# Kernel tuning notes

Measured on AMD Instinct MI355X. Metric: run time of the kernel, lower is better.

Reference implementation:

```python
import jax, jax.numpy as jnp
import numpy as np
from jax import lax

C = 128      # channels
H = 128
W = 128
B = 2
WS = 4       # window size
HEADS = 4
HID = int(C * 2.66)  # 340
EPS = 1e-6


def conv1x1(x, w):
    # x: [b,c,h,w], w: [out,in]
    return jnp.einsum('oc,bchw->bohw', w, x)


def dwconv3(x, w):
    # depthwise 3x3, w: [c,1,3,3]
    return lax.conv_general_dilated(
        x, w, window_strides=(1, 1), padding='SAME',
        feature_group_count=x.shape[1],
        dimension_numbers=('NCHW', 'OIHW', 'NCHW'))


def layernorm(x, w, b):
    # channel-wise LN over dim 1 (per pixel), w/b: [C]
    m = x.mean(axis=1, keepdims=True)
    v = ((x - m) ** 2).mean(axis=1, keepdims=True)
    xn = (x - m) / jnp.sqrt(v + EPS)
    return xn * w[None, :, None, None] + b[None, :, None, None]


def l2norm(x):
    n = jnp.sqrt(jnp.sum(x * x, axis=-1, keepdims=True))
    return x / jnp.maximum(n, 1e-12)


def rsa(x, qkv_w, dw_w, proj_w, temp):
    b, c, h, w = x.shape
    ws = WS
    x_ = jnp.roll(x, (-ws // 2, -ws // 2), axis=(2, 3))  # shifts > 0
    qkv = dwconv3(conv1x1(x_, qkv_w), dw_w)
    q, k, v = jnp.split(qkv, 3, axis=1)

    def win(t):  # b c (h dh) (w dw) -> b (h w) (dh dw) c
        return t.reshape(b, c, h // ws, ws, w // ws, ws) \
                .transpose(0, 2, 4, 3, 5, 1) \
                .reshape(b, (h // ws) * (w // ws), ws * ws, c)

    q, k, v = win(q), win(k), win(v)
    q = l2norm(q)
    k = l2norm(k)
    # attn = q^T @ k  -> [b, nw, c, c]
    attn = jax.nn.relu(jnp.einsum('bnpc,bnpd->bncd', q, k) * temp[0, 0, 0])
    out = jnp.einsum('bnpc,bncd->bnpd', v, attn)  # v @ attn
    out = out.reshape(b, h // ws, w // ws, ws, ws, c) \
             .transpose(0, 5, 1, 3, 2, 4).reshape(b, c, h, w)
    out = jnp.roll(out, (ws // 2, ws // 2), axis=(2, 3))
    return conv1x1(out, proj_w)


def gsa(x, qkv_w, dw_w, proj_w, temp):
    b, c, h, w = x.shape
    hd = HEADS
    ch = c // hd
    qkv = dwconv3(conv1x1(x, qkv_w), dw_w)
    q, k, v = jnp.split(qkv, 3, axis=1)

    def hs(t):  # b (head c) h w -> b head c (h w)
        return t.reshape(b, hd, ch, h * w)

    q, k, v = hs(q), hs(k), hs(v)
    q = l2norm(q)
    k = l2norm(k)
    attn = jax.nn.relu(jnp.einsum('bhcn,bhdn->bhcd', q, k) * temp[0, 0, 0])
    out = jnp.einsum('bhcd,bhdn->bhcn', attn, v).reshape(b, c, h, w)
    return conv1x1(out, proj_w)


def ffn(x, w_in, w_dw, w_out):
    h = dwconv3(conv1x1(x, w_in), w_dw)
    h = jax.nn.gelu(h, approximate=False)
    return conv1x1(h, w_out)


def setup_inputs() -> dict:
    key = jax.random.key(0)
    ks = jax.random.split(key, 16)
    s = 0.05
    d = {
        'x': jax.random.normal(ks[0], (B, C, H, W), jnp.float32),
        # spatial (RSA) branch
        'w_s0': jnp.ones((C,), jnp.float32), 'b_s0': jnp.zeros((C,), jnp.float32),
        'w_s2': jnp.ones((C,), jnp.float32), 'b_s2': jnp.zeros((C,), jnp.float32),
        'rsa_qkv': jax.random.normal(ks[1], (3 * C, C), jnp.float32) * s,
        'rsa_dw': jax.random.normal(ks[2], (3 * C, 1, 3, 3), jnp.float32) * s,
        'rsa_proj': jax.random.normal(ks[3], (C, C), jnp.float32) * s,
        'rsa_temp': jnp.ones((1, 1, 1), jnp.float32),
        'ffs_in': jax.random.normal(ks[4], (HID, C), jnp.float32) * s,
        'ffs_dw': jax.random.normal(ks[5], (HID, 1, 3, 3), jnp.float32) * s,
        'ffs_out': jax.random.normal(ks[6], (C, HID), jnp.float32) * s,
        # channel (GSA) branch
        'w_c0': jnp.ones((C,), jnp.float32), 'b_c0': jnp.zeros((C,), jnp.float32),
        'w_c2': jnp.ones((C,), jnp.float32), 'b_c2': jnp.zeros((C,), jnp.float32),
        'gsa_qkv': jax.random.normal(ks[7], (3 * C, C), jnp.float32) * s,
        'gsa_dw': jax.random.normal(ks[8], (3 * C, 1, 3, 3), jnp.float32) * s,
        'gsa_proj': jax.random.normal(ks[9], (C, C), jnp.float32) * s,
        'gsa_temp': jnp.ones((1, 1, 1), jnp.float32),
        'ffc_in': jax.random.normal(ks[10], (HID, C), jnp.float32) * s,
        'ffc_dw': jax.random.normal(ks[11], (HID, 1, 3, 3), jnp.float32) * s,
        'ffc_out': jax.random.normal(ks[12], (C, HID), jnp.float32) * s,
    }
    return d


def reference(x, w_s0, b_s0, w_s2, b_s2, rsa_qkv, rsa_dw, rsa_proj, rsa_temp,
              ffs_in, ffs_dw, ffs_out,
              w_c0, b_c0, w_c2, b_c2, gsa_qkv, gsa_dw, gsa_proj, gsa_temp,
              ffc_in, ffc_dw, ffc_out):
    # shared_depth = 1: only the i==0 branches execute
    # spatial block (RSA)
    x_ = rsa(layernorm(x, w_s0, b_s0), rsa_qkv, rsa_dw, rsa_proj, rsa_temp)
    x = ffn(layernorm(x_ + x, w_s2, b_s2), ffs_in, ffs_dw, ffs_out) + x_
    # channel block (GSA)
    x_ = gsa(layernorm(x, w_c0, b_c0), gsa_qkv, gsa_dw, gsa_proj, gsa_temp)
    x = ffn(layernorm(x_ + x, w_c2, b_c2), ffc_in, ffc_dw, ffc_out) + x_
    return x
```

## Files before the change

### kernel.cpp

```cpp
#include <hip/hip_runtime.h>
#include <hip/hip_bf16.h>
#include <math.h>

typedef __hip_bfloat16 bf16;
typedef __attribute__((ext_vector_type(8))) short short8;
typedef __attribute__((ext_vector_type(4))) short short4v;
typedef __attribute__((ext_vector_type(4))) float float4v;

static constexpr int cB  = 2;
static constexpr int cC  = 128;
static constexpr int cH  = 128;
static constexpr int cW  = 128;
static constexpr int cP  = cH * cW;
static constexpr int cC3 = 384;
static constexpr int cHID = 340;
static constexpr int cNW = 1024;
static constexpr float cEPS = 1e-6f;

__device__ __forceinline__ float bfu2f(unsigned short u){
  union { unsigned int i; float f; } c; c.i = ((unsigned int)u) << 16; return c.f;
}
__device__ __forceinline__ unsigned short f2b(float f){
  union { float f; unsigned int u; } c; c.f = f;
  unsigned int r = c.u + 0x7FFFu + ((c.u >> 16) & 1u);
  return (unsigned short)(r >> 16);
}

__global__ void k_wcvt(const float* __restrict__ qkv_s, const float* __restrict__ qkv_c,
                       const float* __restrict__ fin_s, const float* __restrict__ fin_c,
                       const float* __restrict__ prj_s, const float* __restrict__ prj_c,
                       const float* __restrict__ fo_s,  const float* __restrict__ fo_c,
                       unsigned short* __restrict__ WB, float* __restrict__ S){
  int i = blockIdx.x * 256 + threadIdx.x;
  if (i >= 319488){
    int j = i - 319488;
    if (j < 8704) S[j] = 0.f;
    return;
  }
  float v;
  if (i < 98304){
    v = (i < 49152) ? qkv_s[i] : qkv_c[i - 49152];
  } else if (i < 196608){
    int j = (i < 147456) ? (i - 98304) : (i - 147456);
    int row = j >> 7, col = j & 127;
    const float* src = (i < 147456) ? fin_s : fin_c;
    v = (row < cHID) ? src[row * 128 + col] : 0.f;
  } else if (i < 229376){
    v = (i < 212992) ? prj_s[i - 196608] : prj_c[i - 212992];
  } else {
    int j = (i < 274432) ? (i - 229376) : (i - 274432);
    int row = j / 352, col = j - row * 352;
    const float* src = (i < 274432) ? fo_s : fo_c;
    v = (col < cHID) ? src[row * cHID + col] : 0.f;
  }
  WB[i] = f2b(v);
}

__global__ void __launch_bounds__(256) k_gemmLN(const unsigned short* __restrict__ Wb,
                                                const float* __restrict__ Xf,
                                                const float* __restrict__ gamma,
                                                const float* __restrict__ beta,
                                                unsigned short* __restrict__ Out){
  __shared__ short Xls[64 * 136];
  __shared__ short Wls[128 * 40];
  __shared__ float gls[128], bls[128];
  __shared__ float psum[64], pssq[64];
  int bid = blockIdx.x;
  int s  = (bid & 7) * 192 + (bid >> 3);
  int mt = s % 3;
  int r3 = s / 3;
  int pt = r3 & 255;
  int b  = r3 >> 8;
  int p0 = pt * 64;
  int m0 = mt * 128;
  int t  = threadIdx.x;
  int px = t & 63, cq = t >> 6;
  if (t < 64){ psum[t] = 0.f; pssq[t] = 0.f; }
  if (t < 128){ gls[t] = gamma[t]; bls[t] = beta[t]; }
  int rh = p0 >> 7, w0 = p0 & 127;
  int hs = (rh + 2) & (cH - 1);
  int sp = hs * cW + ((w0 + 2 + px) & (cW - 1));
  const float* xb = Xf + (size_t)b * cC * cP + sp;
  float xr[32];
  float s1 = 0.f, s2 = 0.f;
  #pragma unroll
  for (int j = 0; j < 32; j++){
    float v = xb[(size_t)(cq * 32 + j) * cP];
    xr[j] = v; s1 += v; s2 += v * v;
  }
  __syncthreads();
  atomicAdd(&psum[px], s1);
  atomicAdd(&pssq[px], s2);
  __syncthreads();
  float mean = psum[px] * (1.f / cC);
  float var  = pssq[px] * (1.f / cC) - mean * mean;
  float rstd = rsqrtf(var + cEPS);
  #pragma unroll
  for (int k = 0; k < 4; k++){
    short8 tv;
    #pragma unroll
    for (int e = 0; e < 8; e++){
      int c = cq * 32 + k * 8 + e;
      tv[e] = (short)f2b((xr[k * 8 + e] - mean) * rstd * gls[c] + bls[c]);
    }
    *(short8*)&Xls[px * 136 + cq * 32 + k * 8] = tv;
  }
  int lanelo = t & 15;
  int quad   = (t >> 4) & 3;
  int wv = t >> 6;
  int w1 = wv & 1;
  int w2 = wv >> 1;
  int srw = t >> 1;
  int kow = (t & 1) * 16;
  float4v acc[2][4];
  #pragma unroll
  for (int i = 0; i < 2; i++)
    #pragma unroll
    for (int j = 0; j < 4; j++)
      acc[i][j] = (float4v){0.f, 0.f, 0.f, 0.f};
  const unsigned short* Wp = Wb + (size_t)(m0 + srw) * 128 + kow;
  short8 a0 = *(const short8*)(Wp);
  short8 a1 = *(const short8*)(Wp + 8);
  for (int k0 = 0; k0 < 128; k0 += 32){
    __syncthreads();
    *(short8*)&Wls[srw * 40 + kow]     = a0;
    *(short8*)&Wls[srw * 40 + kow + 8] = a1;
    __syncthreads();
    if (k0 < 96){
      a0 = *(const short8*)(Wp + k0 + 32);
      a1 = *(const short8*)(Wp + k0 + 40);
    }
    short8 af[2], bfr[4];
    #pragma unroll
    for (int i = 0; i < 2; i++)
      af[i] = *(const short8*)&Xls[(w1 * 32 + i * 16 + lanelo) * 136 + k0 + quad * 8];
    #pragma unroll
    for (int j = 0; j < 4; j++)
      bfr[j] = *(const short8*)&Wls[(w2 * 64 + j * 16 + lanelo) * 40 + quad * 8];
    #pragma unroll
    for (int i = 0; i < 2; i++)
      #pragma unroll
      for (int j = 0; j < 4; j++)
        acc[i][j] = __builtin_amdgcn_mfma_f32_16x16x32_bf16(af[i], bfr[j], acc[i][j], 0, 0, 0);
  }
  __syncthreads();
  #pragma unroll
  for (int i = 0; i < 2; i++)
    #pragma unroll
    for (int j = 0; j < 4; j++){
      int pixloc = w1 * 32 + i * 16 + quad * 4;
      int mloc   = w2 * 64 + j * 16 + lanelo;
      #pragma unroll
      for (int r = 0; r < 4; r++)
        Xls[(pixloc + r) * 136 + mloc] = (short)f2b(acc[i][j][r]);
    }
  __syncthreads();
  unsigned short* Ob = Out + (size_t)b * cP * cC3;
  #pragma unroll
  for (int rr = 0; rr < 4; rr++){
    int id = t + rr * 256;
    int row = id >> 4, col8 = (id & 15) * 8;
    *(short8*)(Ob + (size_t)(p0 + row) * cC3 + m0 + col8) = *(const short8*)&Xls[row * 136 + col8];
  }
}

template<int MODE>
__global__ void __launch_bounds__(256) k_gfuse(const unsigned short* __restrict__ W1,
                                               const unsigned short* __restrict__ Xg,
                                               const float* __restrict__ R,
                                               const float* __restrict__ Base,
                                               const float* __restrict__ gamma,
                                               const float* __restrict__ beta,
                                               float* __restrict__ Tr,
                                               const unsigned short* __restrict__ W2,
                                               unsigned short* __restrict__ Out2,
                                               int K1, int PK1, int PITCH2, int M2LIM){
  __shared__ short XB[64 * 136];
  __shared__ short OB[64 * 136];
  __shared__ float gls[128], bls[128];
  __shared__ float psum[64], pssq[64];
  int b  = blockIdx.z;
  int p0 = blockIdx.x * 64;
  int t  = threadIdx.x;
  int lanelo = t & 15;
  int quad   = (t >> 4) & 3;
  int wv = t >> 6;
  int w2 = wv >> 1, w1 = wv & 1;

  if (t < 128){ gls[t] = gamma[t]; bls[t] = beta[t]; }
  if (t < 64){ psum[t] = 0.f; pssq[t] = 0.f; }

  float4v acc[4][2];
  #pragma unroll
  for (int i = 0; i < 4; i++){
    acc[i][0] = (float4v){0.f, 0.f, 0.f, 0.f};
    acc[i][1] = (float4v){0.f, 0.f, 0.f, 0.f};
  }
  const unsigned short* Wf[4];
  const unsigned short* Xf2[2];
  #pragma unroll
  for (int i = 0; i < 4; i++)
    Wf[i] = W1 + (size_t)(w2 * 64 + i * 16 + lanelo) * K1 + quad * 8;
  #pragma unroll
  for (int j = 0; j < 2; j++)
    Xf2[j] = Xg + (size_t)b * cP * PK1 + (size_t)(p0 + w1 * 32 + j * 16 + lanelo) * PK1 + quad * 8;
  #pragma unroll 2
  for (int k0 = 0; k0 < K1; k0 += 32){
    short8 af[4], bfr[2];
    #pragma unroll
    for (int i = 0; i < 4; i++)
      af[i] = *(const short8*)(Wf[i] + k0);
    #pragma unroll
    for (int j = 0; j < 2; j++)
      bfr[j] = *(const short8*)(Xf2[j] + k0);
    #pragma unroll
    for (int i = 0; i < 4; i++)
      #pragma unroll
      for (int j = 0; j < 2; j++)
        acc[i][j] = __builtin_amdgcn_mfma_f32_16x16x32_bf16(af[i], bfr[j], acc[i][j], 0, 0, 0);
  }
  float lnv[4][2][4];
  #pragma unroll
  for (int i = 0; i < 4; i++)
    #pragma unroll
    for (int j = 0; j < 2; j++){
      int n = p0 + w1 * 32 + j * 16 + lanelo;
      #pragma unroll
      for (int r = 0; r < 4; r++){
        int m = w2 * 64 + i * 16 + quad * 4 + r;
        size_t idx = (size_t)b * cC * cP + (size_t)m * cP + n;
        float v = acc[i][j][r];
        if (MODE == 2) v += R[idx];
        Tr[idx] = v;
        if (MODE == 1) v += Base[idx];
        lnv[i][j][r] = v;
      }
    }
  __syncthreads();
  #pragma unroll
  for (int j = 0; j < 2; j++){
    int nl = w1 * 32 + j * 16 + lanelo;
    float s = 0.f, ss = 0.f;
    #pragma unroll
    for (int i = 0; i < 4; i++)
      #pragma unroll
      for (int r = 0; r < 4; r++){
        float v = lnv[i][j][r];
        s += v; ss += v * v;
      }
    atomicAdd(&psum[nl], s);
    atomicAdd(&pssq[nl], ss);
  }
  __syncthreads();
  #pragma unroll
  for (int j = 0; j < 2; j++){
    int nl = w1 * 32 + j * 16 + lanelo;
    float mean = psum[nl] * (1.f / cC);
    float var = pssq[nl] * (1.f / cC) - mean * mean;
    float rstd = rsqrtf(var + cEPS);
    #pragma unroll
    for (int i = 0; i < 4; i++)
      #pragma unroll
      for (int r = 0; r < 4; r++){
        int m = w2 * 64 + i * 16 + quad * 4 + r;
        XB[nl * 136 + m] = (short)f2b((lnv[i][j][r] - mean) * rstd * gls[m] + bls[m]);
      }
  }
  __syncthreads();
  unsigned short* Ob = Out2 + (size_t)b * cP * PITCH2;
  for (int mc = 0; mc < 3; mc++){
    float4v a2[2][4];
    #pragma unroll
    for (int i = 0; i < 2; i++)
      #pragma unroll
      for (int j = 0; j < 4; j++)
        a2[i][j] = (float4v){0.f, 0.f, 0.f, 0.f};
    #pragma unroll
    for (int k0 = 0; k0 < 128; k0 += 32){
      short8 af2[2], bf2[4];
      #pragma unroll
      for (int i = 0; i < 2; i++)
        af2[i] = *(const short8*)&XB[(w1 * 32 + i * 16 + lanelo) * 136 + k0 + quad * 8];
      #pragma unroll
      for (int j = 0; j < 4; j++)
        bf2[j] = *(const short8*)(W2 + (size_t)(mc * 128 + w2 * 64 + j * 16 + lanelo) * 128 + k0 + quad * 8);
      #pragma unroll
      for (int i = 0; i < 2; i++)
        #pragma unroll
        for (int j = 0; j < 4; j++)
          a2[i][j] = __builtin_amdgcn_mfma_f32_16x16x32_bf16(af2[i], bf2[j], a2[i][j], 0, 0, 0);
    }
    __syncthreads();
    #pragma unroll
    for (int i = 0; i < 2; i++)
      #pragma unroll
      for (int j = 0; j < 4; j++){
        int pixloc = w1 * 32 + i * 16 + quad * 4;
        int mloc   = w2 * 64 + j * 16 + lanelo;
        #pragma unroll
        for (int r = 0; r < 4; r++)
          OB[(pixloc + r) * 136 + mloc] = (short)f2b(a2[i][j][r]);
      }
    __syncthreads();
    #pragma unroll
    for (int rr = 0; rr < 4; rr++){
      int id = t + rr * 256;
      int row = id >> 4, col8 = (id & 15) * 8;
      int wcol = mc * 128 + col8;
      if (wcol < M2LIM)
        *(short8*)(Ob + (size_t)(p0 + row) * PITCH2 + wcol) = *(const short8*)&OB[row * 136 + col8];
    }
  }
}

__global__ void __launch_bounds__(256) k_g64d3(const unsigned short* __restrict__ Wb,
                                               const unsigned short* __restrict__ Xg,
                                               const float* __restrict__ R,
                                               float* __restrict__ Tr,
                                               int K, int PK){
  int b  = blockIdx.z;
  int p0 = blockIdx.x * 64;
  int t  = threadIdx.x;
  int lanelo = t & 15;
  int quad   = (t >> 4) & 3;
  int wv = t >> 6;
  int w2 = wv >> 1, w1 = wv & 1;

  float4v acc[4][2];
  #pragma unroll
  for (int i = 0; i < 4; i++){
    acc[i][0] = (float4v){0.f, 0.f, 0.f, 0.f};
    acc[i][1] = (float4v){0.f, 0.f, 0.f, 0.f};
  }
  const unsigned short* Wf[4];
  const unsigned short* Xf2[2];
  #pragma unroll
  for (int i = 0; i < 4; i++)
    Wf[i] = Wb + (size_t)(w2 * 64 + i * 16 + lanelo) * K + quad * 8;
  #pragma unroll
  for (int j = 0; j < 2; j++)
    Xf2[j] = Xg + (size_t)b * cP * PK + (size_t)(p0 + w1 * 32 + j * 16 + lanelo) * PK + quad * 8;
  #pragma unroll 2
  for (int k0 = 0; k0 < K; k0 += 32){
    short8 af[4], bfr[2];
    #pragma unroll
    for (int i = 0; i < 4; i++)
      af[i] = *(const short8*)(Wf[i] + k0);
    #pragma unroll
    for (int j = 0; j < 2; j++)
      bfr[j] = *(const short8*)(Xf2[j] + k0);
    #pragma unroll
    for (int i = 0; i < 4; i++)
      #pragma unroll
      for (int j = 0; j < 2; j++)
        acc[i][j] = __builtin_amdgcn_mfma_f32_16x16x32_bf16(af[i], bfr[j], acc[i][j], 0, 0, 0);
  }
  #pragma unroll
  for (int i = 0; i < 4; i++)
    #pragma unroll
    for (int j = 0; j < 2; j++){
      int n = p0 + w1 * 32 + j * 16 + lanelo;
      #pragma unroll
      for (int r = 0; r < 4; r++){
        int m = w2 * 64 + i * 16 + quad * 4 + r;
        size_t idx = (size_t)b * cC * cP + (size_t)m * cP + n;
        Tr[idx] = acc[i][j][r] + R[idx];
      }
    }
}

template<int GELU, int CCn, int PITCH>
__global__ void __launch_bounds__(256) k_dw(const unsigned short* __restrict__ in,
                                            const float* __restrict__ wt,
                                            unsigned short* __restrict__ out){
  __shared__ float wls[16 * 76];
  int t = threadIdx.x;
  int cbase = blockIdx.y * 128;
  for (int i = t; i < 16 * 72; i += 256){
    int cg = i / 72, rem = i - cg * 72;
    int tap = rem >> 3, j = rem & 7;
    int c = cbase + cg * 8 + j;
    wls[cg * 76 + rem] = (c < CCn) ? wt[c * 9 + tap] : 0.f;
  }
  __syncthreads();
  int cgl = t & 15, pixl = t >> 4;
  int c0 = cbase + cgl * 8;
  if (c0 >= PITCH) return;
  int p = blockIdx.x * 16 + pixl;
  int h = p >> 7, w = p & 127;
  int b = blockIdx.z;
  const unsigned short* ib = in + (size_t)b * cP * PITCH;
  float4 wreg[18];
  #pragma unroll
  for (int q = 0; q < 18; q++)
    wreg[q] = *(const float4*)&wls[cgl * 76 + q * 4];
  short8 v[9];
  #pragma unroll
  for (int ky = 0; ky < 3; ky++){
    int hh = h + ky - 1;
    bool okh = (unsigned)hh < (unsigned)cH;
    int hc = okh ? hh : h;
    #pragma unroll
    for (int kx = 0; kx < 3; kx++){
      int ww = w + kx - 1;
      bool okw = (unsigned)ww < (unsigned)cW;
      int wc = okw ? ww : w;
      short8 lv = *(const short8*)(ib + (size_t)(hc * cW + wc) * PITCH + c0);
      if (!(okh && okw)) lv = (short8){0,0,0,0,0,0,0,0};
      v[ky * 3 + kx] = lv;
    }
  }
  float acc[8] = {0,0,0,0,0,0,0,0};
  #pragma unroll
  for (int tap = 0; tap < 9; tap++){
    float4 w0 = wreg[tap * 2];
    float4 w1 = wreg[tap * 2 + 1];
    float wa[8] = {w0.x, w0.y, w0.z, w0.w, w1.x, w1.y, w1.z, w1.w};
    #pragma unroll
    for (int j = 0; j < 8; j++)
      acc[j] += wa[j] * bfu2f((unsigned short)v[tap][j]);
  }
  short8 ov;
  #pragma unroll
  for (int j = 0; j < 8; j++){
    float vv = acc[j];
    if (GELU) vv = 0.5f * vv * (1.f + erff(vv * 0.70710678118654752f));
    ov[j] = (short)f2b(vv);
  }
  *(short8*)(out + (size_t)b * cP * PITCH + (size_t)p * PITCH + c0) = ov;
}

__global__ void __launch_bounds__(256) k_rsadw(const unsigned short* __restrict__ qkv,
                                               const float* __restrict__ wt,
                                               const float* __restrict__ temp,
                                               unsigned short* __restrict__ out){
  constexpr int QT = 0;
  constexpr int KT = 5120;
  constexpr int VO = 10240;
  constexpr int HA = 12416;
  constexpr int AT = 12416;
  __shared__ short lds[26528];
  __shared__ float nq[16], nk[16];
  int blk = blockIdx.x;
  int b  = blk >> 10;
  int nw = blk & 1023;
  int hb = nw >> 5, wb = nw & 31;
  int t = threadIdx.x;
  #pragma unroll
  for (int j = 0; j < 5; j++)
    *(short8*)&lds[t * 40 + j * 8] = (short8){0,0,0,0,0,0,0,0};
  if (t < 16) nq[t] = 0.f;
  else if (t < 32) nk[t - 16] = 0.f;
  __syncthreads();
  const unsigned short* base = qkv + (size_t)b * cP * cC3;
  #pragma unroll
  for (int r = 0; r < 7; r++){
    int i = t + 256 * r;
    if (i < 1728){
      int pix6 = i / 48;
      int cg = i - pix6 * 48;
      int hy = pix6 / 6, wx = pix6 - hy * 6;
      int hh = hb * 4 + hy - 1;
      int ww = wb * 4 + wx - 1;
      short8 v = (short8){0,0,0,0,0,0,0,0};
      if ((unsigned)hh < (unsigned)cH && (unsigned)ww < (unsigned)cW)
        v = *(const short8*)(base + (size_t)(hh * cW + ww) * cC3 + cg * 8);
      *(short8*)&lds[HA + pix6 * 392 + cg * 8] = v;
    }
  }
  __syncthreads();
  {
    int px = t & 15, grp = t >> 4;
    int py = px >> 2, pw = px & 3;
    #pragma unroll
    for (int g = 0; g < 3; g++){
      int c0 = grp * 24 + g * 8;
      const float4* wq = (const float4*)(wt + (size_t)c0 * 9);
      float wa[72];
      #pragma unroll
      for (int q = 0; q < 18; q++){
        float4 v4 = wq[q];
        wa[q * 4 + 0] = v4.x; wa[q * 4 + 1] = v4.y;
        wa[q * 4 + 2] = v4.z; wa[q * 4 + 3] = v4.w;
      }
      float acc8[8] = {0,0,0,0,0,0,0,0};
      #pragma unroll
      for (int ky = 0; ky < 3; ky++)
        #pragma unroll
        for (int kx = 0; kx < 3; kx++){
          short8 iv = *(const short8*)&lds[HA + ((py + ky) * 6 + pw + kx) * 392 + c0];
          int tap = ky * 3 + kx;
          #pragma unroll
          for (int e = 0; e < 8; e++)
            acc8[e] += wa[e * 9 + tap] * bfu2f((unsigned short)iv[e]);
        }
      if (c0 < 256){
        int isQ = c0 < 128;
        int off = isQ ? (QT + c0 * 40) : (KT + (c0 - 128) * 40);
        float s = 0.f;
        #pragma unroll
        for (int e = 0; e < 8; e++){
          unsigned short us = f2b(acc8[e]);
          float f = bfu2f(us);
          s += f * f;
          lds[off + e * 40 + px] = (short)us;
        }
        atomicAdd(isQ ? &nq[px] : &nk[px], s);
      } else {
        short8 sv;
        #pragma unroll
        for (int e = 0; e < 8; e++) sv[e] = (short)f2b(acc8[e]);
        *(short8*)&lds[VO + px * 136 + (c0 - 256)] = sv;
      }
    }
  }
  __syncthreads();
  float T = temp[0];
  #pragma unroll
  for (int r = 0; r < 8; r++){
    int idx = t + 256 * r;
    int c = idx >> 4, p = idx & 15;
    float sc = (1.f / fmaxf(sqrtf(nq[p]), 1e-12f)) * (1.f / fmaxf(sqrtf(nk[p]), 1e-12f));
    int a = QT + c * 40 + p;
    lds[a] = (short)f2b(bfu2f((unsigned short)lds[a]) * sc);
  }
  __syncthreads();
  int lanelo = t & 15;
  int quad = (t >> 4) & 3;
  int wv = t >> 6;
  float4v oacc[2];
  oacc[0] = (float4v){0.f,0.f,0.f,0.f};
  oacc[1] = (float4v){0.f,0.f,0.f,0.f};
  for (int ch = 0; ch < 2; ch++){
    #pragma unroll
    for (int ct = 0; ct < 4; ct++){
      int c0 = ch * 64 + ct * 16;
      short8 af = *(const short8*)&lds[QT + (c0 + lanelo) * 40 + quad * 8];
      #pragma unroll
      for (int dt = 0; dt < 2; dt++){
        int d0 = wv * 32 + dt * 16;
        short8 bf = *(const short8*)&lds[KT + (d0 + lanelo) * 40 + quad * 8];
        float4v acc = __builtin_amdgcn_mfma_f32_16x16x32_bf16(af, bf,
                        (float4v){0.f,0.f,0.f,0.f}, 0, 0, 0);
        short4v sv;
        #pragma unroll
        for (int r2 = 0; r2 < 4; r2++) sv[r2] = (short)f2b(fmaxf(acc[r2] * T, 0.f));
        *(short4v*)&lds[AT + (d0 + lanelo) * 72 + ct * 16 + quad * 4] = sv;
      }
    }
    __syncthreads();
    #pragma unroll
    for (int dt = 0; dt < 2; dt++){
      int d0 = wv * 32 + dt * 16;
      #pragma unroll
      for (int kk = 0; kk < 2; kk++){
        short8 av8 = *(const short8*)&lds[VO + lanelo * 136 + ch * 64 + kk * 32 + quad * 8];
        short8 bv8 = *(const short8*)&lds[AT + (d0 + lanelo) * 72 + kk * 32 + quad * 8];
        oacc[dt] = __builtin_amdgcn_mfma_f32_16x16x32_bf16(av8, bv8, oacc[dt], 0, 0, 0);
      }
    }
    __syncthreads();
  }
  #pragma unroll
  for (int dt = 0; dt < 2; dt++){
    int d = wv * 32 + dt * 16 + lanelo;
    #pragma unroll
    for (int r2 = 0; r2 < 4; r2++){
      int p = quad * 4 + r2;
      lds[p * 136 + d] = (short)f2b(oacc[dt][r2]);
    }
  }
  __syncthreads();
  {
    int px = t >> 4, cg = (t & 15) * 8;
    int h2 = (hb * 4 + (px >> 2) + 2) & (cH - 1);
    int w2 = (wb * 4 + (px & 3) + 2) & (cW - 1);
    short8 sv = *(const short8*)&lds[px * 136 + cg];
    *(short8*)(out + (size_t)b * cP * cC + (size_t)(h2 * cW + w2) * cC + cg) = sv;
  }
}

__global__ void __launch_bounds__(256) k_gramdw(const unsigned short* __restrict__ Ain,
                                                const float* __restrict__ dww,
                                                float* __restrict__ S,
                                                float* __restrict__ Qn,
                                                float* __restrict__ Kn){
  __shared__ float qs[32][132];
  __shared__ float ks[32][132];
  __shared__ float wdw[576];
  int blk = blockIdx.x;
  int chunk = blk & 127;
  int bh = blk >> 7;
  int b = bh >> 2, hd = bh & 3;
  int t = threadIdx.x;
  for (int i = t; i < 576; i += 256){
    int lc = i / 9, tpq = i - lc * 9;
    int c = (lc < 32) ? (hd * 32 + lc) : (128 + hd * 32 + (lc - 32));
    wdw[i] = dww[c * 9 + tpq];
  }
  __syncthreads();
  int row = t >> 1;
  int half = t & 1;
  int h = chunk, w = row;
  const unsigned short* Ab = Ain + (size_t)b * cP * cC3;
  float qa[16], ka[16];
  #pragma unroll
  for (int e = 0; e < 16; e++){ qa[e] = 0.f; ka[e] = 0.f; }
  #pragma unroll
  for (int ky = 0; ky < 3; ky++){
    int hh = h + ky - 1;
    if ((unsigned)hh >= (unsigned)cH) continue;
    #pragma unroll
    for (int kx = 0; kx < 3; kx++){
      int ww = w + kx - 1;
      if ((unsigned)ww >= (unsigned)cW) continue;
      const unsigned short* pp = Ab + (size_t)(hh * cW + ww) * cC3 + hd * 32 + half * 16;
      short8 q0 = *(const short8*)pp;
      short8 q1 = *(const short8*)(pp + 8);
      short8 k0v = *(const short8*)(pp + 128);
      short8 k1v = *(const short8*)(pp + 136);
      int tpi = ky * 3 + kx;
      #pragma unroll
      for (int e = 0; e < 8; e++){
        qa[e]     += wdw[(half * 16 + e) * 9 + tpi]          * bfu2f((unsigned short)q0[e]);
        qa[8 + e] += wdw[(half * 16 + 8 + e) * 9 + tpi]      * bfu2f((unsigned short)q1[e]);
        ka[e]     += wdw[(32 + half * 16 + e) * 9 + tpi]     * bfu2f((unsigned short)k0v[e]);
        ka[8 + e] += wdw[(32 + half * 16 + 8 + e) * 9 + tpi] * bfu2f((unsigned short)k1v[e]);
      }
    }
  }
  #pragma unroll
  for (int e = 0; e < 16; e++){
    qs[half * 16 + e][row] = bfu2f(f2b(qa[e]));
    ks[half * 16 + e][row] = bfu2f(f2b(ka[e]));
  }
  __syncthreads();
  if (t < 64){
    const float* rowp = (t < 32) ? qs[t] : ks[t - 32];
    float s = 0.f;
    #pragma unroll
    for (int i = 0; i < 128; i += 4){
      float4 v = *(const float4*)(rowp + i);
      s += v.x*v.x + v.y*v.y + v.z*v.z + v.w*v.w;
    }
    if (t < 32) atomicAdd(&Qn[bh * 32 + t], s);
    else        atomicAdd(&Kn[bh * 32 + (t - 32)], s);
  }
  int cc = (t >> 4) * 2;
  int dd = t & 15;
  float a00 = 0.f, a01 = 0.f, a10 = 0.f, a11 = 0.f;
  for (int n = 0; n < 128; n += 4){
    float4 q0 = *(const float4*)&qs[cc][n];
    float4 q1 = *(const float4*)&qs[cc + 1][n];
    float4 k0 = *(const float4*)&ks[dd][n];
    float4 k1 = *(const float4*)&ks[dd + 16][n];
    a00 += q0.x*k0.x + q0.y*k0.y + q0.z*k0.z + q0.w*k0.w;
    a01 += q0.x*k1.x + q0.y*k1.y + q0.z*k1.z + q0.w*k1.w;
    a10 += q1.x*k0.x + q1.y*k0.y + q1.z*k0.z + q1.w*k0.w;
    a11 += q1.x*k1.x + q1.y*k1.y + q1.z*k1.z + q1.w*k1.w;
  }
  float* Sb = S + (size_t)bh * 1024;
  atomicAdd(&Sb[cc * 32 + dd], a00);
  atomicAdd(&Sb[cc * 32 + dd + 16], a01);
  atomicAdd(&Sb[(cc + 1) * 32 + dd], a10);
  atomicAdd(&Sb[(cc + 1) * 32 + dd + 16], a11);
}

__global__ void __launch_bounds__(256) k_applydw(const unsigned short* __restrict__ Ain,
                                                 const float* __restrict__ dww,
                                                 const float* __restrict__ S,
                                                 const float* __restrict__ Qn,
                                                 const float* __restrict__ Kn,
                                                 const float* __restrict__ temp,
                                                 unsigned short* __restrict__ out){
  __shared__ short atb[128 * 40];
  __shared__ short OT[64 * 136];
  __shared__ float wdw[1152];
  int b = blockIdx.y;
  int nbase = blockIdx.x * 64;
  int t = threadIdx.x;
  float T = temp[0];
  for (int i = t; i < 1152; i += 256)
    wdw[i] = dww[2304 + i];
  #pragma unroll
  for (int it = 0; it < 16; it++){
    int i = t + it * 256;
    int c = i >> 5, d = i & 31;
    int hd = c >> 5, cl = c & 31;
    int bh = b * 4 + hd;
    float nqv = fmaxf(sqrtf(Qn[bh * 32 + cl]), 1e-12f);
    float nkv = fmaxf(sqrtf(Kn[bh * 32 + d]), 1e-12f);
    float v = fmaxf(S[(size_t)bh * 1024 + cl * 32 + d] / (nqv * nkv) * T, 0.f);
    atb[c * 40 + d] = (short)f2b(v);
  }
  __syncthreads();
  int lanelo = t & 15, quad = (t >> 4) & 3, wv = t >> 6;
  int pix = nbase + wv * 16 + lanelo;
  int h = pix >> 7, w = pix & 127;
  const unsigned short* Ab = Ain + (size_t)b * cP * cC3;
  #pragma unroll
  for (int hd = 0; hd < 4; hd++){
    float va[8] = {0,0,0,0,0,0,0,0};
    #pragma unroll
    for (int ky = 0; ky < 3; ky++){
      int hh = h + ky - 1;
      if ((unsigned)hh >= (unsigned)cH) continue;
      #pragma unroll
      for (int kx = 0; kx < 3; kx++){
        int ww = w + kx - 1;
        if ((unsigned)ww >= (unsigned)cW) continue;
        short8 iv = *(const short8*)(Ab + (size_t)(hh * cW + ww) * cC3 + 256 + hd * 32 + quad * 8);
        int tpi = ky * 3 + kx;
        #pragma unroll
        for (int e = 0; e < 8; e++)
          va[e] += wdw[(hd * 32 + quad * 8 + e) * 9 + tpi] * bfu2f((unsigned short)iv[e]);
      }
    }
    short8 af;
    #pragma unroll
    for (int e = 0; e < 8; e++) af[e] = (short)f2b(va[e]);
    #pragma unroll
    for (int cth = 0; cth < 2; cth++){
      int c0 = hd * 32 + cth * 16;
      short8 bf = *(const short8*)&atb[(c0 + lanelo) * 40 + quad * 8];
      float4v acc = __builtin_amdgcn_mfma_f32_16x16x32_bf16(af, bf,
                      (float4v){0.f,0.f,0.f,0.f}, 0, 0, 0);
      #pragma unroll
      for (int r = 0; r < 4; r++)
        OT[(wv * 16 + quad * 4 + r) * 136 + c0 + lanelo] = (short)f2b(acc[r]);
    }
  }
  __syncthreads();
  unsigned short* ob = out + (size_t)b * cP * cC;
  #pragma unroll
  for (int rr = 0; rr < 4; rr++){
    int id = t + rr * 256;
    int row = id >> 4, col8 = (id & 15) * 8;
    *(short8*)(ob + (size_t)(nbase + row) * cC + col8) = *(const short8*)&OT[row * 136 + col8];
  }
}

extern "C" void kernel_launch(void* const* d_in, const int* in_sizes, int n_in,
                              void* d_out, int out_size, void* d_ws, size_t ws_size,
                              hipStream_t stream){
  const float* x     = (const float*)d_in[0];
  const float* w_s0  = (const float*)d_in[1];
  const float* b_s0  = (const float*)d_in[2];
  const float* w_s2  = (const float*)d_in[3];
  const float* b_s2  = (const float*)d_in[4];
  const float* rsa_qkv  = (const float*)d_in[5];
  const float* rsa_dw   = (const float*)d_in[6];
  const float* rsa_proj = (const float*)d_in[7];
  const float* rsa_temp = (const float*)d_in[8];
  const float* ffs_in   = (const float*)d_in[9];
  const float* ffs_dw   = (const float*)d_in[10];
  const float* ffs_out  = (const float*)d_in[11];
  const float* w_c0  = (const float*)d_in[12];
  const float* b_c0  = (const float*)d_in[13];
  const float* w_c2  = (const float*)d_in[14];
  const float* b_c2  = (const float*)d_in[15];
  const float* gsa_qkv  = (const float*)d_in[16];
  const float* gsa_dw   = (const float*)d_in[17];
  const float* gsa_proj = (const float*)d_in[18];
  const float* gsa_temp = (const float*)d_in[19];
  const float* ffc_in   = (const float*)d_in[20];
  const float* ffc_dw   = (const float*)d_in[21];
  const float* ffc_out  = (const float*)d_in[22];

  const size_t szC  = (size_t)cB * cC * cP;
  const size_t szC3 = (size_t)cB * cC3 * cP;
  float* XF = (float*)d_ws;
  float* XS = XF + szC;
  unsigned short* LO   = (unsigned short*)(XS + szC);
  unsigned short* Abuf = LO + szC;
  unsigned short* Bbuf = Abuf + szC3;
  float* S  = (float*)(Bbuf + szC3);
  float* Qn = S + 8192;
  float* Kn = Qn + 256;
  float* AT = Kn + 256;
  unsigned short* WB = (unsigned short*)(AT + 1024);
  unsigned short* W_QKV_S = WB;
  unsigned short* W_QKV_C = WB + 49152;
  unsigned short* W_FIN_S = WB + 98304;
  unsigned short* W_FIN_C = WB + 147456;
  unsigned short* W_PRJ_S = WB + 196608;
  unsigned short* W_PRJ_C = WB + 212992;
  unsigned short* W_FO_S  = WB + 229376;
  unsigned short* W_FO_C  = WB + 274432;

  dim3 t256(256);
  dim3 gG1(cP / 64 * 3 * cB);
  dim3 gG64(cP / 64, 1, cB);
  dim3 gDW(cP / 16, 3, cB);

  k_wcvt<<<dim3(1282), t256, 0, stream>>>(rsa_qkv, gsa_qkv, ffs_in, ffc_in,
                                          rsa_proj, gsa_proj, ffs_out, ffc_out, WB, S);

  k_gemmLN<<<gG1, t256, 0, stream>>>(W_QKV_S, x, w_s0, b_s0, Abuf);
  k_rsadw<<<dim3(cB * cNW), t256, 0, stream>>>(Abuf, rsa_dw, rsa_temp, LO);
  k_gfuse<1><<<gG64, t256, 0, stream>>>(W_PRJ_S, LO, nullptr, x, w_s2, b_s2, XS,
                                        W_FIN_S, Abuf, 128, 128, 352, 352);
  k_dw<1,340,352><<<gDW, t256, 0, stream>>>(Abuf, ffs_dw, Bbuf);
  k_gfuse<2><<<gG64, t256, 0, stream>>>(W_FO_S, Bbuf, XS, nullptr, w_c0, b_c0, XF,
                                        W_QKV_C, Abuf, 352, 352, 384, 384);

  k_gramdw<<<dim3(1024), t256, 0, stream>>>(Abuf, gsa_dw, S, Qn, Kn);
  k_applydw<<<dim3(cP / 64, cB), t256, 0, stream>>>(Abuf, gsa_dw, S, Qn, Kn, gsa_temp, LO);
  k_gfuse<1><<<gG64, t256, 0, stream>>>(W_PRJ_C, LO, nullptr, XF, w_c2, b_c2, XS,
                                        W_FIN_C, Abuf, 128, 128, 352, 352);
  k_dw<1,340,352><<<gDW, t256, 0, stream>>>(Abuf, ffc_dw, Bbuf);
  k_g64d3<<<gG64, t256, 0, stream>>>(W_FO_C, Bbuf, XS, (float*)d_out, 352, 352);
}
```

Baseline: 352.1 us.

## Stage GEMM weight and activation tiles through LDS in fused and residual kernels

```diff
diff --git a/kernel.cpp b/kernel.cpp
--- a/kernel.cpp
+++ b/kernel.cpp
@@ -175,10 +175,12 @@
                                                const unsigned short* __restrict__ W2,
                                                unsigned short* __restrict__ Out2,
                                                int K1, int PK1, int PITCH2, int M2LIM){
+  __shared__ short WA[128 * 136];
+  __shared__ short XA[64 * 136];
   __shared__ short XB[64 * 136];
-  __shared__ short OB[64 * 136];
   __shared__ float gls[128], bls[128];
   __shared__ float psum[64], pssq[64];
+  short* OB = XA;
   int b  = blockIdx.z;
   int p0 = blockIdx.x * 64;
   int t  = threadIdx.x;
@@ -186,6 +188,8 @@
   int quad   = (t >> 4) & 3;
   int wv = t >> 6;
   int w2 = wv >> 1, w1 = wv & 1;
+  int srow = t >> 1, shalf = t & 1;
+  int xrow = t >> 2, xq = t & 3;
 
   if (t < 128){ gls[t] = gamma[t]; bls[t] = beta[t]; }
   if (t < 64){ psum[t] = 0.f; pssq[t] = 0.f; }
@@ -196,28 +200,38 @@
     acc[i][0] = (float4v){0.f, 0.f, 0.f, 0.f};
     acc[i][1] = (float4v){0.f, 0.f, 0.f, 0.f};
   }
-  const unsigned short* Wf[4];
-  const unsigned short* Xf2[2];
-  #pragma unroll
-  for (int i = 0; i < 4; i++)
-    Wf[i] = W1 + (size_t)(w2 * 64 + i * 16 + lanelo) * K1 + quad * 8;
-  #pragma unroll
-  for (int j = 0; j < 2; j++)
-    Xf2[j] = Xg + (size_t)b * cP * PK1 + (size_t)(p0 + w1 * 32 + j * 16 + lanelo) * PK1 + quad * 8;
-  #pragma unroll 2
-  for (int k0 = 0; k0 < K1; k0 += 32){
-    short8 af[4], bfr[2];
-    #pragma unroll
-    for (int i = 0; i < 4; i++)
-      af[i] = *(const short8*)(Wf[i] + k0);
-    #pragma unroll
-    for (int j = 0; j < 2; j++)
-      bfr[j] = *(const short8*)(Xf2[j] + k0);
-    #pragma unroll
-    for (int i = 0; i < 4; i++)
+  const unsigned short* Xbase = Xg + (size_t)b * cP * PK1 + (size_t)(p0 + xrow) * PK1 + xq * 32;
+  const unsigned short* Wbase = W1 + (size_t)srow * K1 + shalf * 64;
+  for (int kb = 0; kb < K1; kb += 128){
+    int CL = K1 - kb; if (CL > 128) CL = 128;
+    __syncthreads();
+    #pragma unroll
+    for (int e = 0; e < 8; e++){
+      int col = shalf * 64 + e * 8;
+      if (col < CL)
+        *(short8*)&WA[srow * 136 + col] = *(const short8*)(Wbase + kb + e * 8);
+    }
+    #pragma unroll
+    for (int e = 0; e < 4; e++){
+      int col = xq * 32 + e * 8;
+      if (col < CL)
+        *(short8*)&XA[xrow * 136 + col] = *(const short8*)(Xbase + kb + e * 8);
+    }
+    __syncthreads();
+    for (int k0 = 0; k0 < CL; k0 += 32){
+      short8 af[4], bfr[2];
+      #pragma unroll
+      for (int i = 0; i < 4; i++)
+        af[i] = *(const short8*)&WA[(w2 * 64 + i * 16 + lanelo) * 136 + k0 + quad * 8];
       #pragma unroll
       for (int j = 0; j < 2; j++)
-        acc[i][j] = __builtin_amdgcn_mfma_f32_16x16x32_bf16(af[i], bfr[j], acc[i][j], 0, 0, 0);
+        bfr[j] = *(const short8*)&XA[(w1 * 32 + j * 16 + lanelo) * 136 + k0 + quad * 8];
+      #pragma unroll
+      for (int i = 0; i < 4; i++)
+        #pragma unroll
+        for (int j = 0; j < 2; j++)
+          acc[i][j] = __builtin_amdgcn_mfma_f32_16x16x32_bf16(af[i], bfr[j], acc[i][j], 0, 0, 0);
+    }
   }
   float lnv[4][2][4];
   #pragma unroll
@@ -266,9 +280,16 @@
         XB[nl * 136 + m] = (short)f2b((lnv[i][j][r] - mean) * rstd * gls[m] + bls[m]);
       }
   }
-  __syncthreads();
   unsigned short* Ob = Out2 + (size_t)b * cP * PITCH2;
   for (int mc = 0; mc < 3; mc++){
+    __syncthreads();
+    {
+      const unsigned short* w2src = W2 + (size_t)(mc * 128 + srow) * 128 + shalf * 64;
+      #pragma unroll
+      for (int e = 0; e < 8; e++)
+        *(short8*)&WA[srow * 136 + shalf * 64 + e * 8] = *(const short8*)(w2src + e * 8);
+    }
+    __syncthreads();
     float4v a2[2][4];
     #pragma unroll
     for (int i = 0; i < 2; i++)
@@ -283,14 +304,13 @@
         af2[i] = *(const short8*)&XB[(w1 * 32 + i * 16 + lanelo) * 136 + k0 + quad * 8];
       #pragma unroll
       for (int j = 0; j < 4; j++)
-        bf2[j] = *(const short8*)(W2 + (size_t)(mc * 128 + w2 * 64 + j * 16 + lanelo) * 128 + k0 + quad * 8);
+        bf2[j] = *(const short8*)&WA[(w2 * 64 + j * 16 + lanelo) * 136 + k0 + quad * 8];
       #pragma unroll
       for (int i = 0; i < 2; i++)
         #pragma unroll
         for (int j = 0; j < 4; j++)
           a2[i][j] = __builtin_amdgcn_mfma_f32_16x16x32_bf16(af2[i], bf2[j], a2[i][j], 0, 0, 0);
     }
-    __syncthreads();
     #pragma unroll
     for (int i = 0; i < 2; i++)
       #pragma unroll
@@ -318,6 +338,8 @@
                                                const float* __restrict__ R,
                                                float* __restrict__ Tr,
                                                int K, int PK){
+  __shared__ short WA[128 * 136];
+  __shared__ short XA[64 * 136];
   int b  = blockIdx.z;
   int p0 = blockIdx.x * 64;
   int t  = threadIdx.x;
@@ -325,6 +347,8 @@
   int quad   = (t >> 4) & 3;
   int wv = t >> 6;
   int w2 = wv >> 1, w1 = wv & 1;
+  int srow = t >> 1, shalf = t & 1;
+  int xrow = t >> 2, xq = t & 3;
 
   float4v acc[4][2];
   #pragma unroll
@@ -332,28 +356,38 @@
     acc[i][0] = (float4v){0.f, 0.f, 0.f, 0.f};
     acc[i][1] = (float4v){0.f, 0.f, 0.f, 0.f};
   }
-  const unsigned short* Wf[4];
-  const unsigned short* Xf2[2];
-  #pragma unroll
-  for (int i = 0; i < 4; i++)
-    Wf[i] = Wb + (size_t)(w2 * 64 + i * 16 + lanelo) * K + quad * 8;
-  #pragma unroll
-  for (int j = 0; j < 2; j++)
-    Xf2[j] = Xg + (size_t)b * cP * PK + (size_t)(p0 + w1 * 32 + j * 16 + lanelo) * PK + quad * 8;
-  #pragma unroll 2
-  for (int k0 = 0; k0 < K; k0 += 32){
-    short8 af[4], bfr[2];
-    #pragma unroll
-    for (int i = 0; i < 4; i++)
-      af[i] = *(const short8*)(Wf[i] + k0);
-    #pragma unroll
-    for (int j = 0; j < 2; j++)
-      bfr[j] = *(const short8*)(Xf2[j] + k0);
-    #pragma unroll
-    for (int i = 0; i < 4; i++)
+  const unsigned short* Xbase = Xg + (size_t)b * cP * PK + (size_t)(p0 + xrow) * PK + xq * 32;
+  const unsigned short* Wbase = Wb + (size_t)srow * K + shalf * 64;
+  for (int kb = 0; kb < K; kb += 128){
+    int CL = K - kb; if (CL > 128) CL = 128;
+    __syncthreads();
+    #pragma unroll
+    for (int e = 0; e < 8; e++){
+      int col = shalf * 64 + e * 8;
+      if (col < CL)
+        *(short8*)&WA[srow * 136 + col] = *(const short8*)(Wbase + kb + e * 8);
+    }
+    #pragma unroll
+    for (int e = 0; e < 4; e++){
+      int col = xq * 32 + e * 8;
+      if (col < CL)
+        *(short8*)&XA[xrow * 136 + col] = *(const short8*)(Xbase + kb + e * 8);
+    }
+    __syncthreads();
+    for (int k0 = 0; k0 < CL; k0 += 32){
+      short8 af[4], bfr[2];
+      #pragma unroll
+      for (int i = 0; i < 4; i++)
+        af[i] = *(const short8*)&WA[(w2 * 64 + i * 16 + lanelo) * 136 + k0 + quad * 8];
       #pragma unroll
       for (int j = 0; j < 2; j++)
-        acc[i][j] = __builtin_amdgcn_mfma_f32_16x16x32_bf16(af[i], bfr[j], acc[i][j], 0, 0, 0);
+        bfr[j] = *(const short8*)&XA[(w1 * 32 + j * 16 + lanelo) * 136 + k0 + quad * 8];
+      #pragma unroll
+      for (int i = 0; i < 4; i++)
+        #pragma unroll
+        for (int j = 0; j < 2; j++)
+          acc[i][j] = __builtin_amdgcn_mfma_f32_16x16x32_bf16(af[i], bfr[j], acc[i][j], 0, 0, 0);
+    }
   }
   #pragma unroll
   for (int i = 0; i < 4; i++)
```

Result: faster. 340.8 us (-3.2%).
